# Kernel tuning notes

Hardware: AMD Instinct MI355X
Metric: run time of the kernel (lower is better)

## Reference

```python
import jax, jax.numpy as jnp
import numpy as np

B, N, DIM = 8, 8192, 512
H, DH = 8, 64
INNER = H * DH
EPS = 1e-5


def setup_inputs() -> dict:
    key = jax.random.key(0)
    ks = jax.random.split(key, 5)
    x = jax.random.normal(ks[0], (B, N, DIM), dtype=jnp.float32)
    w_qkv = jax.random.normal(ks[1], (DIM, 3 * INNER), dtype=jnp.float32) * (DIM ** -0.5)
    ln_w = jnp.ones((INNER,), dtype=jnp.float32)
    ln_b = jnp.zeros((INNER,), dtype=jnp.float32)
    w_out = jax.random.normal(ks[2], (INNER, DIM), dtype=jnp.float32) * (INNER ** -0.5)
    b_out = jnp.zeros((DIM,), dtype=jnp.float32)
    return {"x": x, "w_qkv": w_qkv, "ln_w": ln_w, "ln_b": ln_b,
            "w_out": w_out, "b_out": b_out}


def _layernorm(x, w, b):
    mu = jnp.mean(x, axis=-1, keepdims=True)
    var = jnp.mean(jnp.square(x - mu), axis=-1, keepdims=True)
    return (x - mu) * jax.lax.rsqrt(var + EPS) * w + b


def reference(x, w_qkv, ln_w, ln_b, w_out, b_out):
    b, n, _ = x.shape
    qkv = x @ w_qkv  # [b, n, 3*inner]
    q, k, v = jnp.split(qkv, 3, axis=-1)
    # b n (h d) -> b h n d
    def heads(t):
        return t.reshape(b, n, H, DH).transpose(0, 2, 1, 3)
    q, k, v = heads(q), heads(k), heads(v)
    q = jax.nn.relu(q)
    k = jax.nn.relu(k)
    kv = jnp.einsum('bhnm,bhnd->bhmd', k, v)   # [b, h, d, d]
    out = jnp.einsum('bhnm,bhmd->bhnd', q, kv)  # [b, h, n, d]
    out = out.transpose(0, 2, 1, 3).reshape(b, n, INNER)
    out = _layernorm(out, ln_w, ln_b)
    return out @ w_out + b_out
```

## Files before the change

### kernel.cpp

```cpp
#include <hip/hip_runtime.h>
#include <stdint.h>

#define B_ 8
#define N_ 8192
#define DIM_ 512
#define H_ 8
#define DH_ 64
#define ROWS (B_*N_)
#define TRIPLE (3*DIM_)
#define EPS_ 1e-5f

typedef __attribute__((ext_vector_type(8))) short short8;
typedef __attribute__((ext_vector_type(4))) float f32x4;
typedef __attribute__((ext_vector_type(4))) float fl4;
typedef __attribute__((ext_vector_type(4))) unsigned short us4;
typedef __attribute__((ext_vector_type(8))) unsigned short us8;

#define AS1 __attribute__((address_space(1)))
#define AS3 __attribute__((address_space(3)))

__device__ __forceinline__ void gld16(const void* g, void* l) {
    __builtin_amdgcn_global_load_lds((const AS1 void*)(uintptr_t)g,
                                     (AS3 void*)(unsigned)(uintptr_t)l, 16, 0, 0);
}

__device__ inline unsigned short f2bf(float f) {
    union { float f; unsigned int u; } x; x.f = f;
    unsigned int r = x.u + 0x7fffu + ((x.u >> 16) & 1u);
    return (unsigned short)(r >> 16);
}
__device__ inline float bf2f(unsigned short b) {
    union { unsigned int u; float f; } x; x.u = ((unsigned int)b) << 16;
    return x.f;
}

__device__ __forceinline__ int eoff(int row, int col) {
    return row * 64 + (col ^ ((((unsigned)row >> 2) & 3) << 4));
}

__global__ __launch_bounds__(256) void k_cvt(const float* __restrict__ x,
                                             unsigned short* __restrict__ xb) {
    size_t i = ((size_t)blockIdx.x * 256 + threadIdx.x) * 8;
    fl4 a = *(const fl4*)(x + i);
    fl4 b = *(const fl4*)(x + i + 4);
    us8 r;
    r[0] = f2bf(a[0]); r[1] = f2bf(a[1]); r[2] = f2bf(a[2]); r[3] = f2bf(a[3]);
    r[4] = f2bf(b[0]); r[5] = f2bf(b[1]); r[6] = f2bf(b[2]); r[7] = f2bf(b[3]);
    *(us8*)(xb + i) = r;
}

__global__ void k_prep(const float* __restrict__ w_qkv, const float* __restrict__ w_out,
                       unsigned short* __restrict__ wqkvT, unsigned short* __restrict__ woutT) {
    int idx = blockIdx.x * 256 + threadIdx.x;
    if (idx < TRIPLE * DIM_) {
        int n = idx / DIM_, k = idx - n * DIM_;
        wqkvT[idx] = f2bf(w_qkv[(size_t)k * TRIPLE + n]);
    }
    if (idx < DIM_ * DIM_) {
        int n = idx / DIM_, k = idx - n * DIM_;
        woutT[idx] = f2bf(w_out[(size_t)k * DIM_ + n]);
    }
}

__global__ __launch_bounds__(512, 2) void k_qkv8(const unsigned short* __restrict__ xb,
        const unsigned short* __restrict__ wT,
        unsigned short* __restrict__ qkv)
{
    __shared__ __align__(1024) unsigned short Ab[2][16384];
    __shared__ __align__(1024) unsigned short Bb[2][16384];

    const int tid  = threadIdx.x;
    const int lane = tid & 63;
    const int wid  = tid >> 6;
    const int wr   = wid >> 2;
    const int wc   = wid & 3;
    const int lr   = lane & 15;

    int id  = blockIdx.x;
    int nid = (id & 7) * 192 + (id >> 3);
    int n0  = (nid % 6) * 256;
    int m0  = (nid / 6) * 256;

    const unsigned short* pA[4];
    const unsigned short* pB[4];
    unsigned ldst[4];
#pragma unroll
    for (int j = 0; j < 4; ++j) {
        int s    = tid + j * 512;
        int row  = ((s >> 7) << 4) + ((s >> 2) & 15);
        int colb = ((s & 3) << 4) ^ (((s >> 5) & 1) << 5);
        int col  = ((s >> 6) & 1) * 32 + (colb >> 1);
        pA[j] = xb + (size_t)(m0 + row) * 512 + col;
        pB[j] = wT + (size_t)(n0 + row) * 512 + col;
        ldst[j] = (unsigned)((j * 512 + wid * 64) * 8);
    }
    const int lo = lr * 32 + ((((lane >> 4) << 4) ^ ((lr >> 3) << 5)) >> 1);

    auto STAGE = [&](int t, int c) {
#pragma unroll
        for (int j = 0; j < 4; ++j) {
            gld16(pA[j] + t * 64, (void*)&Ab[c][ldst[j]]);
            gld16(pB[j] + t * 64, (void*)&Bb[c][ldst[j]]);
        }
    };

    f32x4 acc[8][4] = {};
    short8 af[4][2], bf0[2][2], bf1[2][2];

    STAGE(0, 0);
    asm volatile("s_waitcnt vmcnt(0)" ::: "memory");
    __builtin_amdgcn_s_barrier();

    for (int t = 0; t < 8; ++t) {
        const int cur = t & 1;
        const unsigned short* Ac = Ab[cur];
        const unsigned short* Bc = Bb[cur];

        if (t < 7) STAGE(t + 1, cur ^ 1);
#pragma unroll
        for (int m = 0; m < 4; ++m)
#pragma unroll
            for (int ks = 0; ks < 2; ++ks)
                af[m][ks] = *(const short8*)&Ac[(wr * 16 + m * 2 + ks) * 512 + lo];
#pragma unroll
        for (int n = 0; n < 2; ++n)
#pragma unroll
            for (int ks = 0; ks < 2; ++ks)
                bf0[n][ks] = *(const short8*)&Bc[((wc * 4 + n) * 2 + ks) * 512 + lo];
        __builtin_amdgcn_s_barrier();
        __builtin_amdgcn_s_setprio(1);
#pragma unroll
        for (int m = 0; m < 4; ++m)
#pragma unroll
            for (int n = 0; n < 2; ++n)
#pragma unroll
                for (int ks = 0; ks < 2; ++ks)
                    acc[m][n] = __builtin_amdgcn_mfma_f32_16x16x32_bf16(af[m][ks], bf0[n][ks], acc[m][n], 0, 0, 0);
        __builtin_amdgcn_s_setprio(0);
        __builtin_amdgcn_s_barrier();

#pragma unroll
        for (int n = 0; n < 2; ++n)
#pragma unroll
            for (int ks = 0; ks < 2; ++ks)
                bf1[n][ks] = *(const short8*)&Bc[((wc * 4 + 2 + n) * 2 + ks) * 512 + lo];
        __builtin_amdgcn_s_barrier();
        __builtin_amdgcn_s_setprio(1);
#pragma unroll
        for (int m = 0; m < 4; ++m)
#pragma unroll
            for (int n = 0; n < 2; ++n)
#pragma unroll
                for (int ks = 0; ks < 2; ++ks)
                    acc[m][2 + n] = __builtin_amdgcn_mfma_f32_16x16x32_bf16(af[m][ks], bf1[n][ks], acc[m][2 + n], 0, 0, 0);
        __builtin_amdgcn_s_setprio(0);
        __builtin_amdgcn_s_barrier();

#pragma unroll
        for (int m = 0; m < 4; ++m)
#pragma unroll
            for (int ks = 0; ks < 2; ++ks)
                af[m][ks] = *(const short8*)&Ac[(wr * 16 + (4 + m) * 2 + ks) * 512 + lo];
        __builtin_amdgcn_s_barrier();
        __builtin_amdgcn_s_setprio(1);
#pragma unroll
        for (int m = 0; m < 4; ++m)
#pragma unroll
            for (int n = 0; n < 2; ++n)
#pragma unroll
                for (int ks = 0; ks < 2; ++ks)
                    acc[4 + m][2 + n] = __builtin_amdgcn_mfma_f32_16x16x32_bf16(af[m][ks], bf1[n][ks], acc[4 + m][2 + n], 0, 0, 0);
        __builtin_amdgcn_s_setprio(0);
        __builtin_amdgcn_s_barrier();

#pragma unroll
        for (int n = 0; n < 2; ++n)
#pragma unroll
            for (int ks = 0; ks < 2; ++ks)
                bf0[n][ks] = *(const short8*)&Bc[((wc * 4 + n) * 2 + ks) * 512 + lo];
        __builtin_amdgcn_s_barrier();
        __builtin_amdgcn_s_setprio(1);
#pragma unroll
        for (int m = 0; m < 4; ++m)
#pragma unroll
            for (int n = 0; n < 2; ++n)
#pragma unroll
                for (int ks = 0; ks < 2; ++ks)
                    acc[4 + m][n] = __builtin_amdgcn_mfma_f32_16x16x32_bf16(af[m][ks], bf0[n][ks], acc[4 + m][n], 0, 0, 0);
        __builtin_amdgcn_s_setprio(0);
        if (t < 7) asm volatile("s_waitcnt vmcnt(0)" ::: "memory");
        __builtin_amdgcn_s_barrier();
    }

    unsigned short* S = (wid < 4) ? (&Ab[0][0] + wid * 8192)
                                  : (&Bb[0][0] + (wid - 4) * 8192);
    const bool relu_tile = (n0 < 1024);
#pragma unroll
    for (int m = 0; m < 8; ++m) {
        int rbase = m * 16 + ((lane >> 4) << 2);
#pragma unroll
        for (int n = 0; n < 4; ++n) {
            int col = n * 16 + lr;
#pragma unroll
            for (int r = 0; r < 4; ++r) {
                float v = acc[m][n][r];
                if (relu_tile && v < 0.0f) v = 0.0f;
                S[eoff(rbase + r, col)] = f2bf(v);
            }
        }
    }
    __syncthreads();
    {
        int rsub = lane >> 3, sub = lane & 7;
        size_t grow = (size_t)(m0 + wr * 128);
        int gcol = n0 + wc * 64 + sub * 8;
#pragma unroll
        for (int rd = 0; rd < 16; ++rd) {
            int row = rd * 8 + rsub;
            short8 vv = *(const short8*)&S[eoff(row, sub * 8)];
            *(short8*)(qkv + (grow + row) * TRIPLE + gcol) = vv;
        }
    }
}

__global__ __launch_bounds__(256) void k_qkv_f(const float* __restrict__ x,
        const unsigned short* __restrict__ wT,
        unsigned short* __restrict__ qkv)
{
    __shared__ unsigned short As[128][40];
    __shared__ unsigned short Bs[128][40];
    int t = threadIdx.x;
    int lane = t & 63, wave = t >> 6;
    int m0 = blockIdx.y * 128;
    int n0 = blockIdx.x * 128;
    int wm = (wave & 1) * 64, wn = (wave >> 1) * 64;
    int lr = lane & 15, kg = (lane >> 4) * 8;

    f32x4 acc[4][4] = {};
    for (int k0 = 0; k0 < DIM_; k0 += 32) {
#pragma unroll
        for (int i = 0; i < 4; ++i) {
            int c = t + 256 * i;
            int r = c >> 3, c4 = (c & 7) * 4;
            fl4 v = *(const fl4*)(x + (size_t)(m0 + r) * DIM_ + k0 + c4);
            unsigned short* dst = &As[r][c4];
            dst[0] = f2bf(v[0]); dst[1] = f2bf(v[1]); dst[2] = f2bf(v[2]); dst[3] = f2bf(v[3]);
        }
#pragma unroll
        for (int i = 0; i < 2; ++i) {
            int c = t + 256 * i;
            int r = c >> 2, c8 = (c & 3) * 8;
            *(int4*)&Bs[r][c8] = *(const int4*)(wT + (size_t)(n0 + r) * DIM_ + k0 + c8);
        }
        __syncthreads();
        short8 af[4], bfr[4];
#pragma unroll
        for (int i = 0; i < 4; ++i) af[i]  = *(short8*)&As[wm + i*16 + lr][kg];
#pragma unroll
        for (int j = 0; j < 4; ++j) bfr[j] = *(short8*)&Bs[wn + j*16 + lr][kg];
#pragma unroll
        for (int i = 0; i < 4; ++i)
#pragma unroll
            for (int j = 0; j < 4; ++j)
                acc[i][j] = __builtin_amdgcn_mfma_f32_16x16x32_bf16(af[i], bfr[j], acc[i][j], 0, 0, 0);
        __syncthreads();
    }
#pragma unroll
    for (int i = 0; i < 4; ++i) {
        int row = m0 + wm + i*16 + (lane >> 4) * 4;
#pragma unroll
        for (int j = 0; j < 4; ++j) {
            int col = n0 + wn + j*16 + (lane & 15);
            bool rl = (col < 1024);
#pragma unroll
            for (int r = 0; r < 4; ++r) {
                float v = acc[i][j][r];
                if (rl && v < 0.0f) v = 0.0f;
                qkv[(size_t)(row + r) * TRIPLE + col] = f2bf(v);
            }
        }
    }
}

__global__ __launch_bounds__(256) void k_kv(const unsigned short* __restrict__ qkv,
                                            float* __restrict__ kv)
{
    __shared__ unsigned short KT[64][136];
    __shared__ unsigned short VT[64][136];
    __shared__ float red[64 * 64];
    int t = threadIdx.x, lane = t & 63, wave = t >> 6;
    int bh = blockIdx.x;
    int b = bh >> 3, h = bh & 7;
    int chunk = blockIdx.y;
    size_t rowbase = (size_t)b * N_ + (size_t)chunk * 1024;
    int kcol = DIM_ + h * 64;
    int vcol = 2 * DIM_ + h * 64;
    int lr = lane & 15;

    f32x4 acc[4][4] = {};
    for (int tile = 0; tile < 8; ++tile) {
        size_t r0 = rowbase + tile * 128;
#pragma unroll
        for (int i = 0; i < 8; ++i) {
            int c = t + 256 * i;
            int r = c >> 4, f4 = (c & 15) * 4;
            us4 kq = *(const us4*)(qkv + (r0 + r) * TRIPLE + kcol + f4);
            us4 vq = *(const us4*)(qkv + (r0 + r) * TRIPLE + vcol + f4);
#pragma unroll
            for (int j = 0; j < 4; ++j) { KT[f4 + j][r] = kq[j]; VT[f4 + j][r] = vq[j]; }
        }
        __syncthreads();
        int kg = wave * 32 + (lane >> 4) * 8;
        short8 af[4], bfr[4];
#pragma unroll
        for (int i = 0; i < 4; ++i) af[i]  = *(short8*)&KT[i*16 + lr][kg];
#pragma unroll
        for (int j = 0; j < 4; ++j) bfr[j] = *(short8*)&VT[j*16 + lr][kg];
#pragma unroll
        for (int i = 0; i < 4; ++i)
#pragma unroll
            for (int j = 0; j < 4; ++j)
                acc[i][j] = __builtin_amdgcn_mfma_f32_16x16x32_bf16(af[i], bfr[j], acc[i][j], 0, 0, 0);
        __syncthreads();
    }
    for (int w = 0; w < 4; ++w) {
        if (wave == w) {
#pragma unroll
            for (int i = 0; i < 4; ++i)
#pragma unroll
                for (int j = 0; j < 4; ++j)
#pragma unroll
                    for (int r = 0; r < 4; ++r) {
                        int m = i*16 + (lane >> 4) * 4 + r;
                        int d = j*16 + (lane & 15);
                        if (w == 0) red[m * 64 + d] = acc[i][j][r];
                        else        red[m * 64 + d] += acc[i][j][r];
                    }
        }
        __syncthreads();
    }
    float* kvout = kv + (size_t)bh * 4096;
#pragma unroll
    for (int i = 0; i < 16; ++i) {
        int idx = t + 256 * i;
        atomicAdd(&kvout[idx], red[idx]);
    }
}

__global__ __launch_bounds__(256) void k_attn(unsigned short* __restrict__ qkv,
                                              const float* __restrict__ kv)
{
    __shared__ unsigned short Qh[128][72];
    __shared__ unsigned short kvT[64][72];
    __shared__ __align__(64) unsigned short Sout[128 * 64];
    int t = threadIdx.x, lane = t & 63, wave = t >> 6;
    size_t r0 = (size_t)blockIdx.x * 128;
    int b = (int)(r0 / N_);
    int lr = lane & 15;
    for (int h = 0; h < H_; ++h) {
#pragma unroll
        for (int i = 0; i < 8; ++i) {
            int c = t + 256 * i;
            int r = c >> 4, f4 = (c & 15) * 4;
            *(us4*)&Qh[r][f4] = *(const us4*)(qkv + (r0 + r) * TRIPLE + h * 64 + f4);
        }
        const float* kvh = kv + (size_t)(b * 8 + h) * 4096;
#pragma unroll
        for (int i = 0; i < 16; ++i) {
            int idx = t + 256 * i;
            int m = idx >> 6, d = idx & 63;
            kvT[d][m] = f2bf(kvh[idx]);
        }
        __syncthreads();
        f32x4 acc[2][4] = {};
#pragma unroll
        for (int ks = 0; ks < 2; ++ks) {
            int kg = ks * 32 + (lane >> 4) * 8;
            short8 af[2], bfr[4];
#pragma unroll
            for (int i = 0; i < 2; ++i) af[i]  = *(short8*)&Qh[wave*32 + i*16 + lr][kg];
#pragma unroll
            for (int j = 0; j < 4; ++j) bfr[j] = *(short8*)&kvT[j*16 + lr][kg];
#pragma unroll
            for (int i = 0; i < 2; ++i)
#pragma unroll
                for (int j = 0; j < 4; ++j)
                    acc[i][j] = __builtin_amdgcn_mfma_f32_16x16x32_bf16(af[i], bfr[j], acc[i][j], 0, 0, 0);
        }
#pragma unroll
        for (int i = 0; i < 2; ++i)
#pragma unroll
            for (int j = 0; j < 4; ++j) {
                int rbase = wave*32 + i*16 + (lane >> 4) * 4;
                int col = j*16 + lr;
#pragma unroll
                for (int r = 0; r < 4; ++r)
                    Sout[eoff(rbase + r, col)] = f2bf(acc[i][j][r]);
            }
        __syncthreads();
        {
            int sub = t & 7, rsub = t >> 3;
#pragma unroll
            for (int rd = 0; rd < 4; ++rd) {
                int row = rd * 32 + rsub;
                short8 vv = *(const short8*)&Sout[eoff(row, sub * 8)];
                *(short8*)(qkv + (r0 + row) * TRIPLE + h * 64 + sub * 8) = vv;
            }
        }
    }
}

__global__ __launch_bounds__(256) void k_out(const unsigned short* __restrict__ qkv,
        const unsigned short* __restrict__ woutT,
        const float* __restrict__ lnw, const float* __restrict__ lnb,
        const float* __restrict__ bout, float* __restrict__ out)
{
    __shared__ unsigned short As[128][40];
    __shared__ unsigned short Bs[128][40];
    __shared__ float mu[128], rs[128], lw[512], lb[512];
    int t = threadIdx.x, lane = t & 63, wave = t >> 6;
    int m0 = blockIdx.y * 128, n0 = blockIdx.x * 128;
    int wm = (wave & 1) * 64, wn = (wave >> 1) * 64;
    int lr = lane & 15, kg = (lane >> 4) * 8;

    for (int i = t; i < 512; i += 256) { lw[i] = lnw[i]; lb[i] = lnb[i]; }
    {
        int row = t >> 1, half = t & 1;
        const unsigned short* p = qkv + (size_t)(m0 + row) * TRIPLE + half * 256;
        float s = 0.0f, ss = 0.0f;
#pragma unroll 8
        for (int i = 0; i < 64; ++i) {
            us4 v = *(const us4*)(p + i * 4);
#pragma unroll
            for (int j = 0; j < 4; ++j) { float f = bf2f(v[j]); s += f; ss += f * f; }
        }
        s  += __shfl_xor(s, 1);
        ss += __shfl_xor(ss, 1);
        if (half == 0) {
            float m = s * (1.0f / 512.0f);
            float var = ss * (1.0f / 512.0f) - m * m;
            mu[row] = m;
            rs[row] = rsqrtf(var + EPS_);
        }
    }
    __syncthreads();

    f32x4 acc[4][4] = {};
    for (int k0 = 0; k0 < 512; k0 += 32) {
#pragma unroll
        for (int i = 0; i < 4; ++i) {
            int c = t + 256 * i;
            int r = c >> 3, c4 = (c & 7) * 4;
            us4 v = *(const us4*)(qkv + (size_t)(m0 + r) * TRIPLE + k0 + c4);
            float mm = mu[r], rr = rs[r];
            unsigned short* dst = &As[r][c4];
#pragma unroll
            for (int j = 0; j < 4; ++j) {
                float f = (bf2f(v[j]) - mm) * rr * lw[k0 + c4 + j] + lb[k0 + c4 + j];
                dst[j] = f2bf(f);
            }
        }
#pragma unroll
        for (int i = 0; i < 2; ++i) {
            int c = t + 256 * i;
            int r = c >> 2, c8 = (c & 3) * 8;
            *(int4*)&Bs[r][c8] = *(const int4*)(woutT + (size_t)(n0 + r) * DIM_ + k0 + c8);
        }
        __syncthreads();
        short8 af[4], bfr[4];
#pragma unroll
        for (int i = 0; i < 4; ++i) af[i]  = *(short8*)&As[wm + i*16 + lr][kg];
#pragma unroll
        for (int j = 0; j < 4; ++j) bfr[j] = *(short8*)&Bs[wn + j*16 + lr][kg];
#pragma unroll
        for (int i = 0; i < 4; ++i)
#pragma unroll
            for (int j = 0; j < 4; ++j)
                acc[i][j] = __builtin_amdgcn_mfma_f32_16x16x32_bf16(af[i], bfr[j], acc[i][j], 0, 0, 0);
        __syncthreads();
    }
#pragma unroll
    for (int i = 0; i < 4; ++i) {
        int row = m0 + wm + i*16 + (lane >> 4) * 4;
#pragma unroll
        for (int j = 0; j < 4; ++j) {
            int col = n0 + wn + j*16 + (lane & 15);
            float bo = bout[col];
#pragma unroll
            for (int r = 0; r < 4; ++r)
                out[(size_t)(row + r) * DIM_ + col] = acc[i][j][r] + bo;
        }
    }
}

extern "C" void kernel_launch(void* const* d_in, const int* in_sizes, int n_in,
                              void* d_out, int out_size, void* d_ws, size_t ws_size,
                              hipStream_t stream) {
    (void)in_sizes; (void)n_in; (void)out_size;
    const float* x     = (const float*)d_in[0];
    const float* w_qkv = (const float*)d_in[1];
    const float* ln_w  = (const float*)d_in[2];
    const float* ln_b  = (const float*)d_in[3];
    const float* w_out = (const float*)d_in[4];
    const float* b_out = (const float*)d_in[5];
    float* out = (float*)d_out;

    char* ws = (char*)d_ws;
    const size_t QKV_BYTES = (size_t)ROWS * TRIPLE * sizeof(unsigned short);
    const size_t KV_BYTES  = (size_t)64 * 64 * 64 * sizeof(float);
    const size_t WQT_BYTES = (size_t)TRIPLE * DIM_ * sizeof(unsigned short);
    const size_t WOT_BYTES = (size_t)DIM_ * DIM_ * sizeof(unsigned short);
    const size_t XB_BYTES  = (size_t)ROWS * DIM_ * sizeof(unsigned short);
    unsigned short* qkv   = (unsigned short*)ws;
    float*          kvbuf = (float*)(ws + QKV_BYTES);
    unsigned short* wqkvT = (unsigned short*)(ws + QKV_BYTES + KV_BYTES);
    unsigned short* woutT = (unsigned short*)(ws + QKV_BYTES + KV_BYTES + WQT_BYTES);
    unsigned short* xb    = (unsigned short*)(ws + QKV_BYTES + KV_BYTES + WQT_BYTES + WOT_BYTES);
    const size_t NEED = QKV_BYTES + KV_BYTES + WQT_BYTES + WOT_BYTES + XB_BYTES;

    hipMemsetAsync(kvbuf, 0, KV_BYTES, stream);
    k_prep<<<3072, 256, 0, stream>>>(w_qkv, w_out, wqkvT, woutT);
    if (ws_size >= NEED) {
        k_cvt<<<16384, 256, 0, stream>>>(x, xb);
        k_qkv8<<<dim3(1536), 512, 0, stream>>>(xb, wqkvT, qkv);
    } else {
        k_qkv_f<<<dim3(12, 512), 256, 0, stream>>>(x, wqkvT, qkv);
    }
    k_kv<<<dim3(64, 8), 256, 0, stream>>>(qkv, kvbuf);
    k_attn<<<512, 256, 0, stream>>>(qkv, kvbuf);
    k_out<<<dim3(4, 512), 256, 0, stream>>>(qkv, woutT, ln_w, ln_b, b_out, out);
}
```

Before: 570.8 us.

## Fuse LayerNorm into attention kernel epilogue, simplify output GEMM A-load

The attention kernel now keeps all eight heads' outputs for its 128 rows in registers (packed as bf16) and accumulates per-row sum and sum of squares. After the last head it reduces these across lanes, then writes the normalized and affine-transformed values. The output projection kernel therefore loads pre-normalized bf16 with plain 16-byte copies. This removes the per-tile statistics pass and the per-element normalization, which the earlier code repeated for each of the four column blocks. The cost is heavy register use (64 us4 values per thread) and extra barriers in k_attn, which may lower occupancy or cause spills.

Result: slower. 635.5 us (+11.3%).

```diff
diff --git a/kernel.cpp b/kernel.cpp
--- a/kernel.cpp
+++ b/kernel.cpp
@@ -348,15 +348,25 @@
 }
 
 __global__ __launch_bounds__(256) void k_attn(unsigned short* __restrict__ qkv,
-                                              const float* __restrict__ kv)
+                                              const float* __restrict__ kv,
+                                              const float* __restrict__ lnw,
+                                              const float* __restrict__ lnb)
 {
     __shared__ unsigned short Qh[128][72];
     __shared__ unsigned short kvT[64][72];
     __shared__ __align__(64) unsigned short Sout[128 * 64];
+    __shared__ float lwS[512], lbS[512];
     int t = threadIdx.x, lane = t & 63, wave = t >> 6;
     size_t r0 = (size_t)blockIdx.x * 128;
     int b = (int)(r0 / N_);
     int lr = lane & 15;
+
+    for (int i = t; i < 512; i += 256) { lwS[i] = lnw[i]; lbS[i] = lnb[i]; }
+
+    us4 keep[8][2][4];
+    float s8[8] = {}, ss8[8] = {};
+
+#pragma unroll
     for (int h = 0; h < H_; ++h) {
 #pragma unroll
         for (int i = 0; i < 8; ++i) {
@@ -387,15 +397,52 @@
                 for (int j = 0; j < 4; ++j)
                     acc[i][j] = __builtin_amdgcn_mfma_f32_16x16x32_bf16(af[i], bfr[j], acc[i][j], 0, 0, 0);
         }
+        __syncthreads();
+#pragma unroll
+        for (int i = 0; i < 2; ++i)
+#pragma unroll
+            for (int j = 0; j < 4; ++j) {
+                us4 pk;
+#pragma unroll
+                for (int r = 0; r < 4; ++r) {
+                    float v = acc[i][j][r];
+                    s8[i*4+r]  += v;
+                    ss8[i*4+r] += v * v;
+                    pk[r] = f2bf(v);
+                }
+                keep[h][i][j] = pk;
+            }
+    }
+
+    float mu8[8], rs8[8];
+#pragma unroll
+    for (int q = 0; q < 8; ++q) {
+        float s = s8[q], ss = ss8[q];
+        s += __shfl_xor(s, 1);  ss += __shfl_xor(ss, 1);
+        s += __shfl_xor(s, 2);  ss += __shfl_xor(ss, 2);
+        s += __shfl_xor(s, 4);  ss += __shfl_xor(ss, 4);
+        s += __shfl_xor(s, 8);  ss += __shfl_xor(ss, 8);
+        float m = s * (1.0f / 512.0f);
+        mu8[q] = m;
+        rs8[q] = rsqrtf(ss * (1.0f / 512.0f) - m * m + EPS_);
+    }
+
+#pragma unroll
+    for (int h = 0; h < H_; ++h) {
 #pragma unroll
         for (int i = 0; i < 2; ++i)
 #pragma unroll
             for (int j = 0; j < 4; ++j) {
                 int rbase = wave*32 + i*16 + (lane >> 4) * 4;
                 int col = j*16 + lr;
-#pragma unroll
-                for (int r = 0; r < 4; ++r)
-                    Sout[eoff(rbase + r, col)] = f2bf(acc[i][j][r]);
+                float w  = lwS[h*64 + col];
+                float bb = lbS[h*64 + col];
+#pragma unroll
+                for (int r = 0; r < 4; ++r) {
+                    float v = bf2f(keep[h][i][j][r]);
+                    v = (v - mu8[i*4+r]) * rs8[i*4+r] * w + bb;
+                    Sout[eoff(rbase + r, col)] = f2bf(v);
+                }
             }
         __syncthreads();
         {
@@ -407,58 +454,28 @@
                 *(short8*)(qkv + (r0 + row) * TRIPLE + h * 64 + sub * 8) = vv;
             }
         }
+        __syncthreads();
     }
 }
 
 __global__ __launch_bounds__(256) void k_out(const unsigned short* __restrict__ qkv,
         const unsigned short* __restrict__ woutT,
-        const float* __restrict__ lnw, const float* __restrict__ lnb,
         const float* __restrict__ bout, float* __restrict__ out)
 {
     __shared__ unsigned short As[128][40];
     __shared__ unsigned short Bs[128][40];
-    __shared__ float mu[128], rs[128], lw[512], lb[512];
     int t = threadIdx.x, lane = t & 63, wave = t >> 6;
     int m0 = blockIdx.y * 128, n0 = blockIdx.x * 128;
     int wm = (wave & 1) * 64, wn = (wave >> 1) * 64;
     int lr = lane & 15, kg = (lane >> 4) * 8;
 
-    for (int i = t; i < 512; i += 256) { lw[i] = lnw[i]; lb[i] = lnb[i]; }
-    {
-        int row = t >> 1, half = t & 1;
-        const unsigned short* p = qkv + (size_t)(m0 + row) * TRIPLE + half * 256;
-        float s = 0.0f, ss = 0.0f;
-#pragma unroll 8
-        for (int i = 0; i < 64; ++i) {
-            us4 v = *(const us4*)(p + i * 4);
-#pragma unroll
-            for (int j = 0; j < 4; ++j) { float f = bf2f(v[j]); s += f; ss += f * f; }
-        }
-        s  += __shfl_xor(s, 1);
-        ss += __shfl_xor(ss, 1);
-        if (half == 0) {
-            float m = s * (1.0f / 512.0f);
-            float var = ss * (1.0f / 512.0f) - m * m;
-            mu[row] = m;
-            rs[row] = rsqrtf(var + EPS_);
-        }
-    }
-    __syncthreads();
-
     f32x4 acc[4][4] = {};
     for (int k0 = 0; k0 < 512; k0 += 32) {
 #pragma unroll
-        for (int i = 0; i < 4; ++i) {
+        for (int i = 0; i < 2; ++i) {
             int c = t + 256 * i;
-            int r = c >> 3, c4 = (c & 7) * 4;
-            us4 v = *(const us4*)(qkv + (size_t)(m0 + r) * TRIPLE + k0 + c4);
-            float mm = mu[r], rr = rs[r];
-            unsigned short* dst = &As[r][c4];
-#pragma unroll
-            for (int j = 0; j < 4; ++j) {
-                float f = (bf2f(v[j]) - mm) * rr * lw[k0 + c4 + j] + lb[k0 + c4 + j];
-                dst[j] = f2bf(f);
-            }
+            int r = c >> 2, c8 = (c & 3) * 8;
+            *(int4*)&As[r][c8] = *(const int4*)(qkv + (size_t)(m0 + r) * TRIPLE + k0 + c8);
         }
 #pragma unroll
         for (int i = 0; i < 2; ++i) {
@@ -527,6 +544,6 @@
         k_qkv_f<<<dim3(12, 512), 256, 0, stream>>>(x, wqkvT, qkv);
     }
     k_kv<<<dim3(64, 8), 256, 0, stream>>>(qkv, kvbuf);
-    k_attn<<<512, 256, 0, stream>>>(qkv, kvbuf);
-    k_out<<<dim3(4, 512), 256, 0, stream>>>(qkv, woutT, ln_w, ln_b, b_out, out);
-}
+    k_attn<<<512, 256, 0, stream>>>(qkv, kvbuf, ln_w, ln_b);
+    k_out<<<dim3(4, 512), 256, 0, stream>>>(qkv, woutT, b_out, out);
+}
```
